# Performance work log

Measured on AMD Instinct MI355X. Metric: run time of the kernel, lower is better.

The kernel has to match this reference:

```python
import jax, jax.numpy as jnp
import numpy as np

EMBED = 768
HEADS = 12
HEAD_DIM = EMBED // HEADS


def setup_inputs() -> dict:
    key = jax.random.key(0)
    ks = jax.random.split(key, 9)
    B, S, E = 2, 2048, EMBED
    scale = 1.0 / np.sqrt(E)
    return {
        "query": jax.random.normal(ks[0], (B, S, E), jnp.float32),
        "key": jax.random.normal(ks[1], (B, S, E), jnp.float32),
        "value": jax.random.normal(ks[2], (B, S, E), jnp.float32),
        # nn.Linear weights are [out, in]; applied as x @ W.T + b
        "Wq": jax.random.normal(ks[3], (E, E), jnp.float32) * scale,
        "bq": jax.random.normal(ks[4], (E,), jnp.float32) * 0.01,
        "Wk": jax.random.normal(ks[5], (E, E), jnp.float32) * scale,
        "bk": jax.random.normal(ks[6], (E,), jnp.float32) * 0.01,
        "Wv": jax.random.normal(ks[7], (E, E), jnp.float32) * scale,
        "bv": jax.random.normal(ks[8], (E,), jnp.float32) * 0.01,
    }


def reference(query, key, value, Wq, bq, Wk, bk, Wv, bv):
    B, S, E = query.shape
    H, D = HEADS, HEAD_DIM
    # QKV projections (nn.Linear: x @ W.T + b), split into heads
    Q = (query @ Wq.T + bq).reshape(B, S, H, D)
    K = (key @ Wk.T + bk).reshape(B, S, H, D)
    V = (value @ Wv.T + bv).reshape(B, S, H, D)
    # hand-rolled attention: scores -> softmax -> weighted sum
    scores = jnp.einsum("bqhd,bkhd->bhqk", Q, K) / jnp.sqrt(jnp.float32(D))
    attn = jax.nn.softmax(scores, axis=-1)
    out = jnp.einsum("bhqk,bkhd->bqhd", attn, V).reshape(B, S, E)
    return out
```

## Files before the change

kernel.cpp:

```cpp
#include <hip/hip_runtime.h>

#define LOG2E 1.4426950408889634f
#define NEGC (-5.0f * LOG2E)

typedef _Float16 half2v __attribute__((ext_vector_type(2)));
typedef _Float16 half4v __attribute__((ext_vector_type(4)));
typedef _Float16 half8v __attribute__((ext_vector_type(8)));
typedef float float4v __attribute__((ext_vector_type(4)));
typedef float float16v __attribute__((ext_vector_type(16)));
typedef unsigned int uint4v __attribute__((ext_vector_type(4)));

#define NX (2 * 2048 * 768)
#define NW (768 * 768)
#define PO_SPLIT (24 * 2048 * 64)

__device__ __forceinline__ void gload_lds16(const _Float16* g, _Float16* l) {
    __builtin_amdgcn_global_load_lds((const __attribute__((address_space(1))) void*)g,
                                     (__attribute__((address_space(3))) void*)l, 16, 0, 0);
}

__global__ __launch_bounds__(256) void cvt6(
    const float* __restrict__ x0, const float* __restrict__ x1, const float* __restrict__ x2,
    const float* __restrict__ w0, const float* __restrict__ w1, const float* __restrict__ w2,
    _Float16* __restrict__ y0, _Float16* __restrict__ y1, _Float16* __restrict__ y2,
    _Float16* __restrict__ y3, _Float16* __restrict__ y4, _Float16* __restrict__ y5)
{
    const int z = blockIdx.y;
    const float* s; _Float16* d; int n;
    switch (z) {
        case 0: s = x0; d = y0; n = NX; break;
        case 1: s = x1; d = y1; n = NX; break;
        case 2: s = x2; d = y2; n = NX; break;
        case 3: s = w0; d = y3; n = NW; break;
        case 4: s = w1; d = y4; n = NW; break;
        default: s = w2; d = y5; n = NW; break;
    }
    const int i = (blockIdx.x * 256 + threadIdx.x) * 8;
    if (i >= n) return;
    float4v a0 = ((const float4v*)(s + i))[0];
    float4v a1 = ((const float4v*)(s + i))[1];
    half8v h = __builtin_shufflevector(__builtin_convertvector(a0, half4v),
                                       __builtin_convertvector(a1, half4v),
                                       0, 1, 2, 3, 4, 5, 6, 7);
    *(half8v*)(d + i) = h;
}

template<int TM, int TN, int AM, int AN, int MODE>
__device__ __forceinline__ void gemm_body(
    const _Float16* __restrict__ A, const _Float16* __restrict__ B,
    const float* __restrict__ bias, _Float16* __restrict__ O,
    float scale, int m0, int n0, _Float16* At, _Float16* Bt)
{
    const int t    = threadIdx.x;
    const int wave = t >> 6;
    const int lane = t & 63;
    const int quad = lane >> 4;
    const int l16  = lane & 15;
    const int wm   = (wave & 1) * (AM * 16);
    const int wn   = (wave >> 1) * (AN * 16);

    float4v acc[AM][AN];
#pragma unroll
    for (int i = 0; i < AM; i++)
#pragma unroll
        for (int j = 0; j < AN; j++) acc[i][j] = (float4v){0.f, 0.f, 0.f, 0.f};

    const _Float16* Asrc = A + (size_t)m0 * 768;
    const _Float16* Bsrc = B + (size_t)n0 * 768;

    for (int k0 = 0; k0 < 768; k0 += 64) {
#pragma unroll
        for (int j = 0; j < TM / 32; j++) {
            const int s = j * 256 + t;
            const int row = s >> 3;
            const int c = (s & 7) ^ (row & 7);
            gload_lds16(Asrc + (size_t)row * 768 + k0 + c * 8, At + s * 8);
        }
#pragma unroll
        for (int j = 0; j < TN / 32; j++) {
            const int s = j * 256 + t;
            const int row = s >> 3;
            const int c = (s & 7) ^ (row & 7);
            gload_lds16(Bsrc + (size_t)row * 768 + k0 + c * 8, Bt + s * 8);
        }
        __syncthreads();

        half8v af[AM][2], bf[AN][2];
#pragma unroll
        for (int i = 0; i < AM; i++) {
            const int ra = wm + i * 16 + l16;
            const int ca = quad ^ (ra & 7);
            af[i][0] = *(const half8v*)(At + ra * 64 + ca * 8);
            af[i][1] = *(const half8v*)(At + ra * 64 + (ca ^ 4) * 8);
        }
#pragma unroll
        for (int j = 0; j < AN; j++) {
            const int rb = wn + j * 16 + l16;
            const int cb = quad ^ (rb & 7);
            bf[j][0] = *(const half8v*)(Bt + rb * 64 + cb * 8);
            bf[j][1] = *(const half8v*)(Bt + rb * 64 + (cb ^ 4) * 8);
        }
#pragma unroll
        for (int i = 0; i < AM; i++)
#pragma unroll
            for (int j = 0; j < AN; j++) {
                acc[i][j] = __builtin_amdgcn_mfma_f32_16x16x32_f16(af[i][0], bf[j][0], acc[i][j], 0, 0, 0);
                acc[i][j] = __builtin_amdgcn_mfma_f32_16x16x32_f16(af[i][1], bf[j][1], acc[i][j], 0, 0, 0);
            }
        __syncthreads();
    }

    if (MODE == 0) {
#pragma unroll
        for (int j = 0; j < AN; j++) {
            const int col = n0 + wn + j * 16 + l16;
            const float bc = bias[col];
#pragma unroll
            for (int i = 0; i < AM; i++) {
                const int rowb = m0 + wm + i * 16 + quad * 4;
#pragma unroll
                for (int r = 0; r < 4; r++)
                    O[(size_t)(rowb + r) * 768 + col] = (_Float16)((acc[i][j][r] + bc) * scale);
            }
        }
    } else {
#pragma unroll
        for (int i = 0; i < AM; i++) {
#pragma unroll
            for (int r = 0; r < 4; r++) {
                const int m = m0 + wm + i * 16 + quad * 4 + r;
                const float bc = bias[m];
#pragma unroll
                for (int j = 0; j < AN; j++) {
                    const int n = n0 + wn + j * 16 + l16;
                    O[((size_t)(n >> 11) * 768 + m) * 2048 + (n & 2047)] = (_Float16)(acc[i][j][r] + bc);
                }
            }
        }
    }
}

__global__ __launch_bounds__(256) void gemm_all(
    const _Float16* __restrict__ Xq, const _Float16* __restrict__ Xk, const _Float16* __restrict__ Xv,
    const _Float16* __restrict__ Wq, const _Float16* __restrict__ Wk, const _Float16* __restrict__ Wv,
    const float* __restrict__ bq, const float* __restrict__ bk, const float* __restrict__ bv,
    _Float16* __restrict__ Oq, _Float16* __restrict__ Ok, _Float16* __restrict__ Ovt)
{
    __shared__ _Float16 smem[160 * 64];
    const int z = blockIdx.z;
    if (z == 0)
        gemm_body<64, 96, 2, 3, 0>(Xq, Wq, bq, Oq, 0.125f * LOG2E,
                                   blockIdx.x * 64, blockIdx.y * 96, smem, smem + 64 * 64);
    else if (z == 1)
        gemm_body<64, 96, 2, 3, 0>(Xk, Wk, bk, Ok, 1.0f,
                                   blockIdx.x * 64, blockIdx.y * 96, smem, smem + 64 * 64);
    else
        gemm_body<96, 64, 3, 2, 1>(Wv, Xv, bv, Ovt, 1.0f,
                                   blockIdx.y * 96, blockIdx.x * 64, smem, smem + 96 * 64);
}

__global__ __launch_bounds__(256) void attn3(
    const _Float16* __restrict__ Qh,
    const _Float16* __restrict__ Kh,
    const _Float16* __restrict__ Vt,
    _Float16* __restrict__ Po,
    float* __restrict__ lo)
{
    __shared__ _Float16 smem[4][64 * 64];

    const int t    = threadIdx.x;
    const int wave = t >> 6;
    const int lane = t & 63;
    const int hi   = lane >> 5;
    const int l32  = lane & 31;
    const int q0   = blockIdx.x * 128;
    const int bh   = blockIdx.y;
    const int sp   = blockIdx.z;
    const int b    = bh / 12;
    const int h    = bh % 12;
    const int qw   = q0 + wave * 32;

    const _Float16* qp = Qh + (size_t)(b * 2048 + qw + l32) * 768 + h * 64 + hi * 8;
    half8v qf[4];
#pragma unroll
    for (int d = 0; d < 4; d++) qf[d] = *(const half8v*)(qp + d * 16);

    half8v onesA;
#pragma unroll
    for (int j = 0; j < 8; j++) onesA[j] = (_Float16)1.0f;

    float16v ot[2], otl;
#pragma unroll
    for (int dc = 0; dc < 2; dc++)
#pragma unroll
        for (int r = 0; r < 16; r++) ot[dc][r] = 0.f;
#pragma unroll
    for (int r = 0; r < 16; r++) otl[r] = 0.f;

    const _Float16* Kbase = Kh + (size_t)(b * 2048 + sp * 1024) * 768 + h * 64;
    const _Float16* Vbase = Vt + (size_t)(bh * 64) * 2048 + sp * 1024;

    auto stage = [&](int pp, int kt0) {
#pragma unroll
        for (int j = 0; j < 2; j++) {
            const int s = j * 256 + t;
            const int row = s >> 3;
            const int cg = (s & 7) ^ (row & 7);
            gload_lds16(Kbase + (size_t)(kt0 + row) * 768 + cg * 8, &smem[pp][s * 8]);
            gload_lds16(Vbase + (size_t)row * 2048 + kt0 + cg * 8, &smem[2 + pp][s * 8]);
        }
    };

    stage(0, 0);
    int p = 0;

    for (int it = 0; it < 16; it++) {
        __syncthreads();
        if (it < 15) stage(p ^ 1, (it + 1) * 64);

        float16v st[2];
#pragma unroll
        for (int kc = 0; kc < 2; kc++)
#pragma unroll
            for (int r = 0; r < 16; r++) st[kc][r] = 0.f;
#pragma unroll
        for (int ds = 0; ds < 4; ds++) {
#pragma unroll
            for (int kc = 0; kc < 2; kc++) {
                const int row = kc * 32 + l32;
                const int slot = ((ds << 1) | hi) ^ (row & 7);
                half8v kf = *(const half8v*)(&smem[p][row * 64 + slot * 8]);
                st[kc] = __builtin_amdgcn_mfma_f32_32x32x16_f16(kf, qf[ds], st[kc], 0, 0, 0);
            }
        }

        unsigned int pk[2][8];
#pragma unroll
        for (int kc = 0; kc < 2; kc++)
#pragma unroll
            for (int rp = 0; rp < 8; rp++) {
                const float e0 = __builtin_amdgcn_exp2f(st[kc][2 * rp]     + NEGC);
                const float e1 = __builtin_amdgcn_exp2f(st[kc][2 * rp + 1] + NEGC);
                auto hp = __builtin_amdgcn_cvt_pkrtz(e0, e1);
                pk[kc][rp] = __builtin_bit_cast(unsigned int, hp);
            }

#pragma unroll
        for (int ks = 0; ks < 4; ks++) {
            const int kc = ks >> 1;
            const int sb = (ks & 1) * 4;
            const unsigned int d0 = pk[kc][sb], d1 = pk[kc][sb + 1];
            const unsigned int d2 = pk[kc][sb + 2], d3 = pk[kc][sb + 3];
            const unsigned int x = hi ? d0 : d2;
            const unsigned int y = hi ? d1 : d3;
            const unsigned int ex = (unsigned int)__shfl_xor((int)x, 32);
            const unsigned int ey = (unsigned int)__shfl_xor((int)y, 32);
            uint4v bu;
            bu.x = hi ? ex : d0; bu.y = hi ? ey : d1;
            bu.z = hi ? d2 : ex; bu.w = hi ? d3 : ey;
            const half8v pf = __builtin_bit_cast(half8v, bu);
#pragma unroll
            for (int dc = 0; dc < 2; dc++) {
                const int row = dc * 32 + l32;
                const int slot = ((ks << 1) | hi) ^ (row & 7);
                half8v vf = *(const half8v*)(&smem[2 + p][row * 64 + slot * 8]);
                ot[dc] = __builtin_amdgcn_mfma_f32_32x32x16_f16(vf, pf, ot[dc], 0, 0, 0);
            }
            otl = __builtin_amdgcn_mfma_f32_32x32x16_f16(onesA, pf, otl, 0, 0, 0);
        }
        p ^= 1;
    }

    __syncthreads();
    if (hi == 0)
        lo[(size_t)(sp * 24 + bh) * 2048 + qw + l32] = otl[0];

    float* fo = (float*)(&smem[0][0]) + wave * 2048;
#pragma unroll
    for (int dc = 0; dc < 2; dc++)
#pragma unroll
        for (int g = 0; g < 4; g++) {
            float4v v;
#pragma unroll
            for (int r = 0; r < 4; r++) v[r] = ot[dc][4 * g + r];
            const int c = dc * 8 + 2 * g + hi;
            const int cs = c ^ (l32 & 15);
            *(float4v*)(fo + l32 * 64 + cs * 4) = v;
        }
    const int r4 = lane >> 4, li = lane & 15;
    _Float16* prow = Po + (size_t)(sp * 24 + bh) * 2048 * 64 + (size_t)qw * 64;
#pragma unroll
    for (int pass = 0; pass < 8; pass++) {
        const int qq = pass * 4 + r4;
        float4v v = *(const float4v*)(fo + qq * 64 + (li ^ (qq & 15)) * 4);
        *(half4v*)(prow + (size_t)qq * 64 + li * 4) = __builtin_convertvector(v, half4v);
    }
}

__global__ __launch_bounds__(256) void combine2(
    const _Float16* __restrict__ Po, const float* __restrict__ lo,
    float* __restrict__ out)
{
    const int tid = blockIdx.x * 256 + threadIdx.x;
    const int idx = tid * 4;
    const int d = idx & 63;
    const int r = idx >> 6;
    const int h = r % 12;
    const int t2 = r / 12;
    const int q = t2 & 2047;
    const int b = t2 >> 11;
    const int bh = b * 12 + h;

    const size_t pbase = ((size_t)bh * 2048 + q) * 64 + d;
    float4v p0 = __builtin_convertvector(*(const half4v*)(Po + pbase), float4v);
    float4v p1 = __builtin_convertvector(*(const half4v*)(Po + PO_SPLIT + pbase), float4v);
    const float l0 = lo[(size_t)bh * 2048 + q];
    const float l1 = lo[24 * 2048 + (size_t)bh * 2048 + q];
    const float inv = 1.0f / (l0 + l1);
    float4v v;
#pragma unroll
    for (int i = 0; i < 4; i++) v[i] = (p0[i] + p1[i]) * inv;
    *(float4v*)(out + idx) = v;
}

extern "C" void kernel_launch(void* const* d_in, const int* in_sizes, int n_in,
                              void* d_out, int out_size, void* d_ws, size_t ws_size,
                              hipStream_t stream) {
    const float* q  = (const float*)d_in[0];
    const float* k  = (const float*)d_in[1];
    const float* v  = (const float*)d_in[2];
    const float* Wq = (const float*)d_in[3];
    const float* bq = (const float*)d_in[4];
    const float* Wk = (const float*)d_in[5];
    const float* bk = (const float*)d_in[6];
    const float* Wv = (const float*)d_in[7];
    const float* bv = (const float*)d_in[8];
    float* out = (float*)d_out;

    _Float16* ws   = (_Float16*)d_ws;
    _Float16* Qh   = ws;
    _Float16* Kh   = Qh + NX;
    _Float16* Vth  = Kh + NX;
    _Float16* Xq16 = Vth + NX;
    _Float16* Xk16 = Xq16 + NX;
    _Float16* Xv16 = Xk16 + NX;
    _Float16* Wq16 = Xv16 + NX;
    _Float16* Wk16 = Wq16 + NW;
    _Float16* Wv16 = Wk16 + NW;
    _Float16* Po   = Xq16;
    float*    lo   = (float*)(Po + 2 * PO_SPLIT);

    cvt6<<<dim3(1536, 6), 256, 0, stream>>>(q, k, v, Wq, Wk, Wv,
                                            Xq16, Xk16, Xv16, Wq16, Wk16, Wv16);
    gemm_all<<<dim3(64, 8, 3), 256, 0, stream>>>(
        Xq16, Xk16, Xv16, Wq16, Wk16, Wv16, bq, bk, bv, Qh, Kh, Vth);
    attn3<<<dim3(16, 24, 2), 256, 0, stream>>>(Qh, Kh, Vth, Po, lo);
    combine2<<<dim3(3072), 256, 0, stream>>>(Po, lo, out);
}
```

Measured before the change: 170.2 us.

## Split attention KV into four chunks, enlarge GEMM tiles, flatten conversion grid

The attention kernel now splits the key/value range into four chunks of 512 instead of two of 1024, doubling the block count to fill more compute units. Split 0 writes its unnormalized fp32 partial straight into the output, and the combine kernel adds the other three fp16 partials and divides by the summed row sums. The QKV GEMM tiles grow from 64 to 128 along the sequence dimension to improve operand reuse. The conversion kernel uses a flat 1D grid so no threads idle past the end of the smaller weight tensors. The cost is more partial-result traffic and combine reads, plus fewer GEMM blocks.

```diff
diff --git a/kernel.cpp b/kernel.cpp
--- a/kernel.cpp
+++ b/kernel.cpp
@@ -22,27 +22,31 @@
 __global__ __launch_bounds__(256) void cvt6(
     const float* __restrict__ x0, const float* __restrict__ x1, const float* __restrict__ x2,
     const float* __restrict__ w0, const float* __restrict__ w1, const float* __restrict__ w2,
-    _Float16* __restrict__ y0, _Float16* __restrict__ y1, _Float16* __restrict__ y2,
-    _Float16* __restrict__ y3, _Float16* __restrict__ y4, _Float16* __restrict__ y5)
-{
-    const int z = blockIdx.y;
-    const float* s; _Float16* d; int n;
-    switch (z) {
-        case 0: s = x0; d = y0; n = NX; break;
-        case 1: s = x1; d = y1; n = NX; break;
-        case 2: s = x2; d = y2; n = NX; break;
-        case 3: s = w0; d = y3; n = NW; break;
-        case 4: s = w1; d = y4; n = NW; break;
-        default: s = w2; d = y5; n = NW; break;
-    }
-    const int i = (blockIdx.x * 256 + threadIdx.x) * 8;
-    if (i >= n) return;
-    float4v a0 = ((const float4v*)(s + i))[0];
-    float4v a1 = ((const float4v*)(s + i))[1];
+    _Float16* __restrict__ yx, _Float16* __restrict__ yw)
+{
+    const size_t gi = ((size_t)blockIdx.x * 256 + threadIdx.x) * 8;
+    const float* s;
+    _Float16* d;
+    size_t off;
+    if (gi < (size_t)3 * NX) {
+        const int z = (int)(gi / NX);
+        off = gi - (size_t)z * NX;
+        s = (z == 0) ? x0 : (z == 1) ? x1 : x2;
+        d = yx + (size_t)z * NX;
+    } else {
+        const size_t gj = gi - (size_t)3 * NX;
+        if (gj >= (size_t)3 * NW) return;
+        const int z = (int)(gj / NW);
+        off = gj - (size_t)z * NW;
+        s = (z == 0) ? w0 : (z == 1) ? w1 : w2;
+        d = yw + (size_t)z * NW;
+    }
+    float4v a0 = ((const float4v*)(s + off))[0];
+    float4v a1 = ((const float4v*)(s + off))[1];
     half8v h = __builtin_shufflevector(__builtin_convertvector(a0, half4v),
                                        __builtin_convertvector(a1, half4v),
                                        0, 1, 2, 3, 4, 5, 6, 7);
-    *(half8v*)(d + i) = h;
+    *(half8v*)(d + off) = h;
 }
 
 template<int TM, int TN, int AM, int AN, int MODE>
@@ -146,25 +150,26 @@
     const float* __restrict__ bq, const float* __restrict__ bk, const float* __restrict__ bv,
     _Float16* __restrict__ Oq, _Float16* __restrict__ Ok, _Float16* __restrict__ Ovt)
 {
-    __shared__ _Float16 smem[160 * 64];
+    __shared__ _Float16 smem[224 * 64];
     const int z = blockIdx.z;
     if (z == 0)
-        gemm_body<64, 96, 2, 3, 0>(Xq, Wq, bq, Oq, 0.125f * LOG2E,
-                                   blockIdx.x * 64, blockIdx.y * 96, smem, smem + 64 * 64);
+        gemm_body<128, 96, 4, 3, 0>(Xq, Wq, bq, Oq, 0.125f * LOG2E,
+                                    blockIdx.x * 128, blockIdx.y * 96, smem, smem + 128 * 64);
     else if (z == 1)
-        gemm_body<64, 96, 2, 3, 0>(Xk, Wk, bk, Ok, 1.0f,
-                                   blockIdx.x * 64, blockIdx.y * 96, smem, smem + 64 * 64);
+        gemm_body<128, 96, 4, 3, 0>(Xk, Wk, bk, Ok, 1.0f,
+                                    blockIdx.x * 128, blockIdx.y * 96, smem, smem + 128 * 64);
     else
-        gemm_body<96, 64, 3, 2, 1>(Wv, Xv, bv, Ovt, 1.0f,
-                                   blockIdx.y * 96, blockIdx.x * 64, smem, smem + 96 * 64);
-}
-
-__global__ __launch_bounds__(256) void attn3(
+        gemm_body<96, 128, 3, 4, 1>(Wv, Xv, bv, Ovt, 1.0f,
+                                    blockIdx.y * 96, blockIdx.x * 128, smem, smem + 96 * 64);
+}
+
+__global__ __launch_bounds__(256) void attn4(
     const _Float16* __restrict__ Qh,
     const _Float16* __restrict__ Kh,
     const _Float16* __restrict__ Vt,
     _Float16* __restrict__ Po,
-    float* __restrict__ lo)
+    float* __restrict__ lo,
+    float* __restrict__ out)
 {
     __shared__ _Float16 smem[4][64 * 64];
 
@@ -197,8 +202,8 @@
 #pragma unroll
     for (int r = 0; r < 16; r++) otl[r] = 0.f;
 
-    const _Float16* Kbase = Kh + (size_t)(b * 2048 + sp * 1024) * 768 + h * 64;
-    const _Float16* Vbase = Vt + (size_t)(bh * 64) * 2048 + sp * 1024;
+    const _Float16* Kbase = Kh + (size_t)(b * 2048 + sp * 512) * 768 + h * 64;
+    const _Float16* Vbase = Vt + (size_t)(bh * 64) * 2048 + sp * 512;
 
     auto stage = [&](int pp, int kt0) {
 #pragma unroll
@@ -214,9 +219,9 @@
     stage(0, 0);
     int p = 0;
 
-    for (int it = 0; it < 16; it++) {
+    for (int it = 0; it < 8; it++) {
         __syncthreads();
-        if (it < 15) stage(p ^ 1, (it + 1) * 64);
+        if (it < 7) stage(p ^ 1, (it + 1) * 64);
 
         float16v st[2];
 #pragma unroll
@@ -288,16 +293,26 @@
             *(float4v*)(fo + l32 * 64 + cs * 4) = v;
         }
     const int r4 = lane >> 4, li = lane & 15;
-    _Float16* prow = Po + (size_t)(sp * 24 + bh) * 2048 * 64 + (size_t)qw * 64;
-#pragma unroll
-    for (int pass = 0; pass < 8; pass++) {
-        const int qq = pass * 4 + r4;
-        float4v v = *(const float4v*)(fo + qq * 64 + (li ^ (qq & 15)) * 4);
-        *(half4v*)(prow + (size_t)qq * 64 + li * 4) = __builtin_convertvector(v, half4v);
-    }
-}
-
-__global__ __launch_bounds__(256) void combine2(
+    if (sp == 0) {
+        float* orow = out + (size_t)(b * 2048 + qw) * 768 + h * 64;
+#pragma unroll
+        for (int pass = 0; pass < 8; pass++) {
+            const int qq = pass * 4 + r4;
+            float4v v = *(const float4v*)(fo + qq * 64 + (li ^ (qq & 15)) * 4);
+            *(float4v*)(orow + (size_t)qq * 768 + li * 4) = v;
+        }
+    } else {
+        _Float16* prow = Po + (size_t)((sp - 1) * 24 + bh) * 2048 * 64 + (size_t)qw * 64;
+#pragma unroll
+        for (int pass = 0; pass < 8; pass++) {
+            const int qq = pass * 4 + r4;
+            float4v v = *(const float4v*)(fo + qq * 64 + (li ^ (qq & 15)) * 4);
+            *(half4v*)(prow + (size_t)qq * 64 + li * 4) = __builtin_convertvector(v, half4v);
+        }
+    }
+}
+
+__global__ __launch_bounds__(256) void combine4(
     const _Float16* __restrict__ Po, const float* __restrict__ lo,
     float* __restrict__ out)
 {
@@ -312,14 +327,21 @@
     const int bh = b * 12 + h;
 
     const size_t pbase = ((size_t)bh * 2048 + q) * 64 + d;
-    float4v p0 = __builtin_convertvector(*(const half4v*)(Po + pbase), float4v);
-    float4v p1 = __builtin_convertvector(*(const half4v*)(Po + PO_SPLIT + pbase), float4v);
-    const float l0 = lo[(size_t)bh * 2048 + q];
-    const float l1 = lo[24 * 2048 + (size_t)bh * 2048 + q];
-    const float inv = 1.0f / (l0 + l1);
+    float4v acc = *(const float4v*)(out + idx);
+#pragma unroll
+    for (int s = 0; s < 3; s++) {
+        float4v ps = __builtin_convertvector(
+            *(const half4v*)(Po + (size_t)s * PO_SPLIT + pbase), float4v);
+#pragma unroll
+        for (int i = 0; i < 4; i++) acc[i] += ps[i];
+    }
+    float l = 0.f;
+#pragma unroll
+    for (int s = 0; s < 4; s++) l += lo[(size_t)(s * 24 + bh) * 2048 + q];
+    const float inv = 1.0f / l;
     float4v v;
 #pragma unroll
-    for (int i = 0; i < 4; i++) v[i] = (p0[i] + p1[i]) * inv;
+    for (int i = 0; i < 4; i++) v[i] = acc[i] * inv;
     *(float4v*)(out + idx) = v;
 }
 
@@ -341,19 +363,15 @@
     _Float16* Qh   = ws;
     _Float16* Kh   = Qh + NX;
     _Float16* Vth  = Kh + NX;
-    _Float16* Xq16 = Vth + NX;
-    _Float16* Xk16 = Xq16 + NX;
-    _Float16* Xv16 = Xk16 + NX;
-    _Float16* Wq16 = Xv16 + NX;
-    _Float16* Wk16 = Wq16 + NW;
-    _Float16* Wv16 = Wk16 + NW;
-    _Float16* Po   = Xq16;
-    float*    lo   = (float*)(Po + 2 * PO_SPLIT);
-
-    cvt6<<<dim3(1536, 6), 256, 0, stream>>>(q, k, v, Wq, Wk, Wv,
-                                            Xq16, Xk16, Xv16, Wq16, Wk16, Wv16);
-    gemm_all<<<dim3(64, 8, 3), 256, 0, stream>>>(
-        Xq16, Xk16, Xv16, Wq16, Wk16, Wv16, bq, bk, bv, Qh, Kh, Vth);
-    attn3<<<dim3(16, 24, 2), 256, 0, stream>>>(Qh, Kh, Vth, Po, lo);
-    combine2<<<dim3(3072), 256, 0, stream>>>(Po, lo, out);
-}
+    _Float16* X16  = Vth + NX;
+    _Float16* W16  = X16 + 3 * NX;
+    _Float16* Po   = X16;
+    float*    lo   = (float*)(Po + 3 * PO_SPLIT);
+
+    cvt6<<<dim3(5472), 256, 0, stream>>>(q, k, v, Wq, Wk, Wv, X16, W16);
+    gemm_all<<<dim3(32, 8, 3), 256, 0, stream>>>(
+        X16, X16 + NX, X16 + 2 * NX, W16, W16 + NW, W16 + 2 * NW,
+        bq, bk, bv, Qh, Kh, Vth);
+    attn4<<<dim3(16, 24, 4), 256, 0, stream>>>(Qh, Kh, Vth, Po, lo, out);
+    combine4<<<dim3(3072), 256, 0, stream>>>(Po, lo, out);
+}
```

Result: no change. 171.8 us (+1.0%).
